# Optimization experiments

Hardware: AMD Instinct MI355X
Metric: run time of the kernel (lower is better)

## Reference

```python
import jax, jax.numpy as jnp
import numpy as np

N_NODES = 10000
N_EDGES = 320000
D_FEAT = 128          # per-node feature dim -> in_dim = 2*D_FEAT = 256
OUT_DIM = 128
SCALES = 3


def setup_inputs() -> dict:
    key = jax.random.key(0)
    ks = jax.random.split(key, 7)
    node_features = jax.random.normal(ks[0], (N_NODES, D_FEAT), dtype=jnp.float32)
    temporal_info = jax.random.normal(ks[1], (N_NODES,), dtype=jnp.float32)
    in_dim_p1 = 2 * D_FEAT + 1  # 257: concat(src, dest) + temporal gap
    W1 = jax.random.normal(ks[2], (SCALES, in_dim_p1, OUT_DIM), dtype=jnp.float32) * 0.05
    b1 = jax.random.normal(ks[3], (SCALES, OUT_DIM), dtype=jnp.float32) * 0.05
    W2 = jax.random.normal(ks[4], (SCALES, OUT_DIM, OUT_DIM), dtype=jnp.float32) * 0.05
    b2 = jax.random.normal(ks[5], (SCALES, OUT_DIM), dtype=jnp.float32) * 0.05
    edge_index = jax.random.randint(ks[6], (2, N_EDGES), 0, N_NODES, dtype=jnp.int64)
    return {
        "node_features": node_features,
        "temporal_info": temporal_info,
        "W1": W1, "b1": b1, "W2": W2, "b2": b2,
        "edge_index": edge_index,
    }


def reference(node_features, temporal_info, W1, b1, W2, b2, edge_index):
    src, dest = edge_index[0], edge_index[1]
    # gather node pairs + temporal gap -> [E, 2*D+1]
    gap = (temporal_info[src] - temporal_info[dest])[:, None]
    edge_features = jnp.concatenate(
        [node_features[src], node_features[dest], gap], axis=-1)
    # all scales' 2-layer MLPs in one batched einsum; s = scale axis
    h = jax.nn.relu(jnp.einsum('ef,sfo->seo', edge_features, W1) + b1[:, None, :])
    tokens = jnp.einsum('seo,sop->sep', h, W2) + b2[:, None, :]  # [S, E, OUT]
    return tokens.mean(axis=0)  # mean over scales -> [E, OUT]
```

## Files before the change

kernel.cpp:

```cpp
#include <hip/hip_runtime.h>
#include <stdint.h>

#define NN 10000
#define NE 320000
#define DF 128
#define OD 128
#define NS 3

typedef __attribute__((ext_vector_type(8))) short bf16x8;
typedef __attribute__((ext_vector_type(16))) float f32x16;

static __device__ __forceinline__ uint32_t f2bf(float f) {
  uint32_t u = __float_as_uint(f);
  return (u + 0x7FFFu + ((u >> 16) & 1u)) >> 16;
}
static __device__ __forceinline__ float bflo(uint32_t u) { return __uint_as_float(u << 16); }
static __device__ __forceinline__ float bfhi(uint32_t u) { return __uint_as_float(u & 0xFFFF0000u); }

static __device__ __forceinline__ uint32_t relu2(uint32_t a, uint32_t d) {
  float f0 = fmaxf(bflo(a) + bflo(d), 0.0f);
  float f1 = fmaxf(bfhi(a) + bfhi(d), 0.0f);
  return f2bf(f0) | (f2bf(f1) << 16);
}

__global__ __launch_bounds__(256) void prep_w2(
    const float* __restrict__ W2, const float* __restrict__ b2,
    unsigned short* __restrict__ w2t, float* __restrict__ bmean)
{
  int tid = blockIdx.x * 256 + threadIdx.x;
  if (tid < NS * OD * OD) {
    int s = tid / (OD * OD);
    int r = tid % (OD * OD);
    int k = r / OD;
    int n = r % OD;
    w2t[(s * OD + n) * OD + k] = (unsigned short)f2bf(W2[tid]);
  }
  if (tid < OD) bmean[tid] = (b2[tid] + b2[OD + tid] + b2[2 * OD + tid]) * (1.0f / 3.0f);
}

__global__ __launch_bounds__(256) void node_proj(
    const float* __restrict__ nf, const float* __restrict__ temporal,
    const float* __restrict__ W1, const float* __restrict__ b1,
    unsigned short* __restrict__ Qsrc, unsigned short* __restrict__ Qdst)
{
  __shared__ unsigned short Asm[8 * 64 * 8];
  __shared__ unsigned short Bsm[4 * 8 * 64 * 8];
  __shared__ float tsh[32];

  const int t = threadIdx.x;
  const int c = blockIdx.y;
  const int s = c >> 1, proj = c & 1;

  {
    int o = t & 127, qh = t >> 7;
    const float* wbase = W1 + (size_t)(s * 257 + proj * 128) * OD + o;
    int nt = o >> 5, lnlo = o & 31;
    #pragma unroll
    for (int r = 0; r < 8; r++) {
      int kh = qh * 8 + r;
      float v[8];
      #pragma unroll
      for (int j = 0; j < 8; j++) v[j] = wbase[(size_t)(kh * 8 + j) * OD];
      uint32_t pk[4];
      #pragma unroll
      for (int i = 0; i < 4; i++) pk[i] = f2bf(v[2 * i]) | (f2bf(v[2 * i + 1]) << 16);
      int q = kh >> 1, half = kh & 1;
      uint32_t* d = (uint32_t*)(Bsm + ((nt * 8 + q) * 64 + half * 32 + lnlo) * 8);
      d[0] = pk[0]; d[1] = pk[1]; d[2] = pk[2]; d[3] = pk[3];
    }
  }

  const int lane = t & 63, w = t >> 6;
  const int o = w * 32 + (lane & 31);
  const float w1gv = W1[(size_t)(s * 257 + 256) * OD + o];
  const float b1v = b1[s * OD + o];
  unsigned short* Qt = (proj == 0) ? Qsrc : Qdst;
  const int m = t >> 3, j16 = t & 7;

  for (int it = 0; it < 8; it++) {
    const int m0 = (blockIdx.x * 8 + it) * 32;
    if (m0 >= NN) break;

    if (t < 32) tsh[t] = (m0 + t < NN) ? temporal[m0 + t] : 0.0f;

    {
      int node = m0 + m;
      float v[16];
      if (node < NN) {
        const float4* p = (const float4*)(nf + (size_t)node * DF + j16 * 16);
        #pragma unroll
        for (int i = 0; i < 4; i++) {
          float4 x = p[i];
          v[4 * i] = x.x; v[4 * i + 1] = x.y; v[4 * i + 2] = x.z; v[4 * i + 3] = x.w;
        }
      } else {
        #pragma unroll
        for (int i = 0; i < 16; i++) v[i] = 0.0f;
      }
      uint32_t pk[8];
      #pragma unroll
      for (int i = 0; i < 8; i++) pk[i] = f2bf(v[2 * i]) | (f2bf(v[2 * i + 1]) << 16);
      uint32_t* d0 = (uint32_t*)(Asm + (j16 * 64 + (m ^ j16)) * 8);
      uint32_t* d1 = (uint32_t*)(Asm + (j16 * 64 + ((32 + m) ^ j16)) * 8);
      d0[0] = pk[0]; d0[1] = pk[1]; d0[2] = pk[2]; d0[3] = pk[3];
      d1[0] = pk[4]; d1[1] = pk[5]; d1[2] = pk[6]; d1[3] = pk[7];
    }
    __syncthreads();

    f32x16 C;
    #pragma unroll
    for (int i = 0; i < 16; i++) C[i] = 0.0f;
    #pragma unroll
    for (int q = 0; q < 8; q++) {
      bf16x8 a = *(const bf16x8*)(Asm + (q * 64 + (lane ^ q)) * 8);
      bf16x8 b = *(const bf16x8*)(Bsm + ((w * 8 + q) * 64 + lane) * 8);
      C = __builtin_amdgcn_mfma_f32_32x32x16_bf16(a, b, C, 0, 0, 0);
    }

    #pragma unroll
    for (int r = 0; r < 16; r++) {
      int row = (r & 3) + 8 * (r >> 2) + 4 * (lane >> 5);
      int node = m0 + row;
      if (node < NN) {
        float val = C[r];
        if (proj == 0) val += b1v + tsh[row] * w1gv;
        else           val -= tsh[row] * w1gv;
        Qt[(size_t)node * (NS * OD) + s * OD + o] = (unsigned short)f2bf(val);
      }
    }
    __syncthreads();
  }
}

__global__ __launch_bounds__(256) void edge_mlp(
    const unsigned short* __restrict__ Qsrc, const unsigned short* __restrict__ Qdst,
    const unsigned short* __restrict__ W2T, const float* __restrict__ bmean,
    const int* __restrict__ ei, float* __restrict__ out)
{
  __shared__ unsigned short hsm[NS * 8 * 64 * 8];

  const int t = threadIdx.x;
  const int lane = t & 63, w = t >> 6;
  const int nlo = lane & 31, khi = lane >> 5;

  bf16x8 bfrag[NS][8];
  {
    int n = w * 32 + nlo;
    #pragma unroll
    for (int s = 0; s < NS; s++) {
      const unsigned short* base = W2T + ((s * OD + n) * OD + khi * 8);
      #pragma unroll
      for (int q = 0; q < 8; q++)
        bfrag[s][q] = *(const bf16x8*)(base + q * 16);
    }
  }
  const float bmv = bmean[w * 32 + nlo];

  const int m = t >> 3, j16 = t & 7;

  int sn[4], dn[4];
  #pragma unroll
  for (int tt = 0; tt < 4; tt++) {
    int e = blockIdx.x * 128 + tt * 32 + m;
    sn[tt] = ei[e];
    dn[tt] = ei[NE + e];
  }

  uint4 G[12], G2[12];
  {
    const unsigned short* ps = Qsrc + (size_t)sn[0] * (NS * OD) + j16 * 16;
    const unsigned short* pd = Qdst + (size_t)dn[0] * (NS * OD) + j16 * 16;
    #pragma unroll
    for (int s = 0; s < NS; s++) {
      G[4 * s + 0] = *(const uint4*)(ps + s * OD);
      G[4 * s + 1] = *(const uint4*)(ps + s * OD + 8);
      G[4 * s + 2] = *(const uint4*)(pd + s * OD);
      G[4 * s + 3] = *(const uint4*)(pd + s * OD + 8);
    }
  }

  #pragma unroll
  for (int tt = 0; tt < 4; tt++) {
    const int e0 = blockIdx.x * 128 + tt * 32;

    #pragma unroll
    for (int s = 0; s < NS; s++) {
      uint4 a0 = G[4 * s + 0], a1 = G[4 * s + 1];
      uint4 d0 = G[4 * s + 2], d1 = G[4 * s + 3];
      uint4 w0, w1;
      w0.x = relu2(a0.x, d0.x); w0.y = relu2(a0.y, d0.y);
      w0.z = relu2(a0.z, d0.z); w0.w = relu2(a0.w, d0.w);
      w1.x = relu2(a1.x, d1.x); w1.y = relu2(a1.y, d1.y);
      w1.z = relu2(a1.z, d1.z); w1.w = relu2(a1.w, d1.w);
      *(uint4*)(hsm + ((s * 8 + j16) * 64 + (m ^ j16)) * 8) = w0;
      *(uint4*)(hsm + ((s * 8 + j16) * 64 + ((32 + m) ^ j16)) * 8) = w1;
    }

    if (tt < 3) {
      const unsigned short* ps = Qsrc + (size_t)sn[tt + 1] * (NS * OD) + j16 * 16;
      const unsigned short* pd = Qdst + (size_t)dn[tt + 1] * (NS * OD) + j16 * 16;
      #pragma unroll
      for (int s = 0; s < NS; s++) {
        G2[4 * s + 0] = *(const uint4*)(ps + s * OD);
        G2[4 * s + 1] = *(const uint4*)(ps + s * OD + 8);
        G2[4 * s + 2] = *(const uint4*)(pd + s * OD);
        G2[4 * s + 3] = *(const uint4*)(pd + s * OD + 8);
      }
    }
    __syncthreads();

    f32x16 C;
    #pragma unroll
    for (int i = 0; i < 16; i++) C[i] = 0.0f;
    #pragma unroll
    for (int s = 0; s < NS; s++) {
      #pragma unroll
      for (int q = 0; q < 8; q++) {
        bf16x8 a = *(const bf16x8*)(hsm + ((s * 8 + q) * 64 + (lane ^ q)) * 8);
        C = __builtin_amdgcn_mfma_f32_32x32x16_bf16(a, bfrag[s][q], C, 0, 0, 0);
      }
    }

    #pragma unroll
    for (int r = 0; r < 16; r++) {
      int row = (r & 3) + 8 * (r >> 2) + 4 * khi;
      out[(size_t)(e0 + row) * OD + w * 32 + nlo] = C[r] * (1.0f / 3.0f) + bmv;
    }
    __syncthreads();

    #pragma unroll
    for (int i = 0; i < 12; i++) G[i] = G2[i];
  }
}

extern "C" void kernel_launch(void* const* d_in, const int* in_sizes, int n_in,
                              void* d_out, int out_size, void* d_ws, size_t ws_size,
                              hipStream_t stream) {
  const float* nf       = (const float*)d_in[0];
  const float* temporal = (const float*)d_in[1];
  const float* W1       = (const float*)d_in[2];
  const float* b1       = (const float*)d_in[3];
  const float* W2       = (const float*)d_in[4];
  const float* b2       = (const float*)d_in[5];
  const int*   ei       = (const int*)d_in[6];
  float* out = (float*)d_out;

  char* ws = (char*)d_ws;
  unsigned short* Qsrc = (unsigned short*)ws;
  unsigned short* Qdst = (unsigned short*)(ws + 7680000);
  unsigned short* W2T  = (unsigned short*)(ws + 15360000);
  float*          bmv  = (float*)(ws + 15360000 + 98304);

  prep_w2 <<<dim3(192),    dim3(256), 0, stream>>>(W2, b2, W2T, bmv);
  node_proj<<<dim3(40, 6), dim3(256), 0, stream>>>(nf, temporal, W1, b1, Qsrc, Qdst);
  edge_mlp <<<dim3(2500),  dim3(256), 0, stream>>>(Qsrc, Qdst, W2T, bmv, ei, out);
}
```

Before: 266.2 us.

## Make edge MLP persistent with double-buffered LDS and deeper gather pipeline

The edge kernel now launches 500 blocks that each loop over 20 tiles of 32 edges, instead of 2500 blocks each handling 4 tiles. The hidden-activation LDS buffer is double-buffered, so the next tile's relu/pack can be written while the MFMAs read the current one, with a single lightweight barrier per step. Edge indices are prefetched two tiles ahead and node rows one tile ahead. The W2 fragment load is amortized over more tiles per block. It also raises wave priority around the MFMA section and uses nontemporal stores for the output. The costs are higher register and LDS pressure and fewer blocks for latency hiding.

New measurement: 294.4 us. 1.11x slower.

```diff
diff --git a/kernel.cpp b/kernel.cpp
--- a/kernel.cpp
+++ b/kernel.cpp
@@ -21,6 +21,11 @@
   float f0 = fmaxf(bflo(a) + bflo(d), 0.0f);
   float f1 = fmaxf(bfhi(a) + bfhi(d), 0.0f);
   return f2bf(f0) | (f2bf(f1) << 16);
+}
+
+static __device__ __forceinline__ void lds_barrier() {
+  asm volatile("s_waitcnt lgkmcnt(0)" ::: "memory");
+  __builtin_amdgcn_s_barrier();
 }
 
 __global__ __launch_bounds__(256) void prep_w2(
@@ -132,12 +137,47 @@
   }
 }
 
+#define EGRID 500
+#define ENT   20
+
+static __device__ __forceinline__ void gather12(
+    uint4* G, const unsigned short* __restrict__ Qsrc,
+    const unsigned short* __restrict__ Qdst, int sn, int dn, int j16)
+{
+  const unsigned short* ps = Qsrc + (size_t)sn * (NS * OD) + j16 * 16;
+  const unsigned short* pd = Qdst + (size_t)dn * (NS * OD) + j16 * 16;
+  #pragma unroll
+  for (int s = 0; s < NS; s++) {
+    G[4 * s + 0] = *(const uint4*)(ps + s * OD);
+    G[4 * s + 1] = *(const uint4*)(ps + s * OD + 8);
+    G[4 * s + 2] = *(const uint4*)(pd + s * OD);
+    G[4 * s + 3] = *(const uint4*)(pd + s * OD + 8);
+  }
+}
+
+static __device__ __forceinline__ void produce_h(
+    unsigned short* HS, const uint4* G, int m, int j16)
+{
+  #pragma unroll
+  for (int s = 0; s < NS; s++) {
+    uint4 a0 = G[4 * s + 0], a1 = G[4 * s + 1];
+    uint4 d0 = G[4 * s + 2], d1 = G[4 * s + 3];
+    uint4 w0, w1;
+    w0.x = relu2(a0.x, d0.x); w0.y = relu2(a0.y, d0.y);
+    w0.z = relu2(a0.z, d0.z); w0.w = relu2(a0.w, d0.w);
+    w1.x = relu2(a1.x, d1.x); w1.y = relu2(a1.y, d1.y);
+    w1.z = relu2(a1.z, d1.z); w1.w = relu2(a1.w, d1.w);
+    *(uint4*)(HS + ((s * 8 + j16) * 64 + (m ^ j16)) * 8) = w0;
+    *(uint4*)(HS + ((s * 8 + j16) * 64 + ((32 + m) ^ j16)) * 8) = w1;
+  }
+}
+
 __global__ __launch_bounds__(256) void edge_mlp(
     const unsigned short* __restrict__ Qsrc, const unsigned short* __restrict__ Qdst,
     const unsigned short* __restrict__ W2T, const float* __restrict__ bmean,
     const int* __restrict__ ei, float* __restrict__ out)
 {
-  __shared__ unsigned short hsm[NS * 8 * 64 * 8];
+  __shared__ unsigned short hsm[2][NS * 8 * 64 * 8];
 
   const int t = threadIdx.x;
   const int lane = t & 63, w = t >> 6;
@@ -155,82 +195,53 @@
     }
   }
   const float bmv = bmean[w * 32 + nlo];
-
   const int m = t >> 3, j16 = t & 7;
 
-  int sn[4], dn[4];
-  #pragma unroll
-  for (int tt = 0; tt < 4; tt++) {
-    int e = blockIdx.x * 128 + tt * 32 + m;
-    sn[tt] = ei[e];
-    dn[tt] = ei[NE + e];
-  }
-
-  uint4 G[12], G2[12];
-  {
-    const unsigned short* ps = Qsrc + (size_t)sn[0] * (NS * OD) + j16 * 16;
-    const unsigned short* pd = Qdst + (size_t)dn[0] * (NS * OD) + j16 * 16;
-    #pragma unroll
-    for (int s = 0; s < NS; s++) {
-      G[4 * s + 0] = *(const uint4*)(ps + s * OD);
-      G[4 * s + 1] = *(const uint4*)(ps + s * OD + 8);
-      G[4 * s + 2] = *(const uint4*)(pd + s * OD);
-      G[4 * s + 3] = *(const uint4*)(pd + s * OD + 8);
-    }
-  }
-
-  #pragma unroll
-  for (int tt = 0; tt < 4; tt++) {
-    const int e0 = blockIdx.x * 128 + tt * 32;
-
-    #pragma unroll
-    for (int s = 0; s < NS; s++) {
-      uint4 a0 = G[4 * s + 0], a1 = G[4 * s + 1];
-      uint4 d0 = G[4 * s + 2], d1 = G[4 * s + 3];
-      uint4 w0, w1;
-      w0.x = relu2(a0.x, d0.x); w0.y = relu2(a0.y, d0.y);
-      w0.z = relu2(a0.z, d0.z); w0.w = relu2(a0.w, d0.w);
-      w1.x = relu2(a1.x, d1.x); w1.y = relu2(a1.y, d1.y);
-      w1.z = relu2(a1.z, d1.z); w1.w = relu2(a1.w, d1.w);
-      *(uint4*)(hsm + ((s * 8 + j16) * 64 + (m ^ j16)) * 8) = w0;
-      *(uint4*)(hsm + ((s * 8 + j16) * 64 + ((32 + m) ^ j16)) * 8) = w1;
-    }
-
-    if (tt < 3) {
-      const unsigned short* ps = Qsrc + (size_t)sn[tt + 1] * (NS * OD) + j16 * 16;
-      const unsigned short* pd = Qdst + (size_t)dn[tt + 1] * (NS * OD) + j16 * 16;
-      #pragma unroll
-      for (int s = 0; s < NS; s++) {
-        G2[4 * s + 0] = *(const uint4*)(ps + s * OD);
-        G2[4 * s + 1] = *(const uint4*)(ps + s * OD + 8);
-        G2[4 * s + 2] = *(const uint4*)(pd + s * OD);
-        G2[4 * s + 3] = *(const uint4*)(pd + s * OD + 8);
-      }
-    }
-    __syncthreads();
-
-    f32x16 C;
-    #pragma unroll
-    for (int i = 0; i < 16; i++) C[i] = 0.0f;
-    #pragma unroll
-    for (int s = 0; s < NS; s++) {
-      #pragma unroll
-      for (int q = 0; q < 8; q++) {
-        bf16x8 a = *(const bf16x8*)(hsm + ((s * 8 + q) * 64 + (lane ^ q)) * 8);
-        C = __builtin_amdgcn_mfma_f32_32x32x16_bf16(a, bfrag[s][q], C, 0, 0, 0);
-      }
-    }
-
-    #pragma unroll
-    for (int r = 0; r < 16; r++) {
-      int row = (r & 3) + 8 * (r >> 2) + 4 * khi;
-      out[(size_t)(e0 + row) * OD + w * 32 + nlo] = C[r] * (1.0f / 3.0f) + bmv;
-    }
-    __syncthreads();
-
-    #pragma unroll
-    for (int i = 0; i < 12; i++) G[i] = G2[i];
-  }
+  auto EB = [&](int k) -> int {
+    int kk = (k < ENT) ? k : (ENT - 1);
+    return (blockIdx.x + (kk >> 2) * EGRID) * 128 + (kk & 3) * 32;
+  };
+
+  int sn, dn;
+  uint4 GA[12], GB[12];
+
+  { int e = EB(0) + m; sn = ei[e]; dn = ei[NE + e]; }
+  gather12(GB, Qsrc, Qdst, sn, dn, j16);
+  { int e = EB(1) + m; sn = ei[e]; dn = ei[NE + e]; }
+  gather12(GA, Qsrc, Qdst, sn, dn, j16);
+  { int e = EB(2) + m; sn = ei[e]; dn = ei[NE + e]; }
+  produce_h(hsm[0], GB, m, j16);
+  lds_barrier();
+
+#define STEP(K, GC, GN, P) do {                                               \
+    if ((K) + 2 < ENT) gather12(GN, Qsrc, Qdst, sn, dn, j16);                 \
+    { int e3 = EB((K) + 3) + m; sn = ei[e3]; dn = ei[NE + e3]; }              \
+    f32x16 C;                                                                 \
+    _Pragma("unroll") for (int i = 0; i < 16; i++) C[i] = 0.0f;               \
+    __builtin_amdgcn_s_setprio(1);                                            \
+    _Pragma("unroll") for (int s = 0; s < NS; s++) {                          \
+      _Pragma("unroll") for (int q = 0; q < 8; q++) {                         \
+        bf16x8 a = *(const bf16x8*)(hsm[P] + ((s * 8 + q) * 64 + (lane ^ q)) * 8); \
+        C = __builtin_amdgcn_mfma_f32_32x32x16_bf16(a, bfrag[s][q], C, 0, 0, 0);   \
+      }                                                                       \
+    }                                                                         \
+    __builtin_amdgcn_s_setprio(0);                                            \
+    if ((K) + 1 < ENT) produce_h(hsm[(P) ^ 1], GC, m, j16);                   \
+    const int e0 = EB(K);                                                     \
+    _Pragma("unroll") for (int r = 0; r < 16; r++) {                          \
+      int row = (r & 3) + 8 * (r >> 2) + 4 * khi;                             \
+      __builtin_nontemporal_store(C[r] * (1.0f / 3.0f) + bmv,                 \
+          &out[(size_t)(e0 + row) * OD + w * 32 + nlo]);                      \
+    }                                                                         \
+    lds_barrier();                                                            \
+  } while (0)
+
+  #pragma unroll 1
+  for (int kk = 0; kk < ENT; kk += 2) {
+    STEP(kk,     GA, GB, 0);
+    STEP(kk + 1, GB, GA, 1);
+  }
+#undef STEP
 }
 
 extern "C" void kernel_launch(void* const* d_in, const int* in_sizes, int n_in,
@@ -251,7 +262,7 @@
   unsigned short* W2T  = (unsigned short*)(ws + 15360000);
   float*          bmv  = (float*)(ws + 15360000 + 98304);
 
-  prep_w2 <<<dim3(192),    dim3(256), 0, stream>>>(W2, b2, W2T, bmv);
-  node_proj<<<dim3(40, 6), dim3(256), 0, stream>>>(nf, temporal, W1, b1, Qsrc, Qdst);
-  edge_mlp <<<dim3(2500),  dim3(256), 0, stream>>>(Qsrc, Qdst, W2T, bmv, ei, out);
-}
+  prep_w2 <<<dim3(192),     dim3(256), 0, stream>>>(W2, b2, W2T, bmv);
+  node_proj<<<dim3(40, 6),  dim3(256), 0, stream>>>(nf, temporal, W1, b1, Qsrc, Qdst);
+  edge_mlp <<<dim3(EGRID),  dim3(256), 0, stream>>>(Qsrc, Qdst, W2T, bmv, ei, out);
+}
```
